# Performance work log

Measured on AMD Instinct MI355X. Metric: run time of the kernel, lower is better.

The kernel has to match this reference:

```python
import jax, jax.numpy as jnp
import numpy as np

B, S, H, T = 64, 512, 768, 400


def setup_inputs() -> dict:
    key = jax.random.key(0)
    k1, k2 = jax.random.split(key)
    hidden = jax.random.normal(k1, (B, S, H), dtype=jnp.float32)
    # word_ids: non-decreasing piece->word map per sample, like HF tokenizer word_ids()
    word_ids = jnp.sort(jax.random.randint(k2, (B, S), 0, T), axis=-1).astype(jnp.int32)
    return {"hidden": hidden, "word_ids": word_ids, "num_tokens": T}


def reference(hidden, word_ids, num_tokens):
    # Ragged segment mean-pool: pool subword pieces into per-word reps.
    # hidden: [B, S, H] float; word_ids: [B, S] int in [0, num_tokens)
    b, s, h = hidden.shape
    # Flatten (sample, word) into one global segment id: sample*T + word
    seg = (jnp.arange(b, dtype=word_ids.dtype)[:, None] * num_tokens + word_ids).reshape(-1)
    sums = jax.ops.segment_sum(hidden.reshape(b * s, h), seg, num_segments=b * num_tokens)
    counts = jax.ops.segment_sum(jnp.ones((b * s,), hidden.dtype), seg, num_segments=b * num_tokens)
    # Words with zero pieces -> sum 0 / 1 = 0, matching torch.zeros fallback
    pooled = sums / jnp.maximum(counts, 1.0)[:, None]
    return pooled.reshape(b, num_tokens, h)
```

## Files before the change

kernel.cpp:

```cpp
#include <hip/hip_runtime.h>


#define BB 64
#define SS 512
#define HH 768
#define TT 400
#define TCHUNK 16
#define NCHUNK (TT / TCHUNK)

__global__ __launch_bounds__(256) void bert_lattice_pool_kernel(
    const float* __restrict__ hidden,
    const int* __restrict__ word_ids,
    float* __restrict__ out)
{
    __shared__ int wid[SS];
    __shared__ int sstart[TCHUNK];
    __shared__ int send[TCHUNK];

    const int blk = blockIdx.x;
    const int b   = blk / NCHUNK;
    const int t0  = (blk - b * NCHUNK) * TCHUNK;

    const int tid = threadIdx.x;

    {
        const int2* src = reinterpret_cast<const int2*>(word_ids + b * SS);
        reinterpret_cast<int2*>(wid)[tid] = src[tid];
    }
    if (tid < TCHUNK) { sstart[tid] = 0; send[tid] = 0; }
    __syncthreads();

    #pragma unroll
    for (int k = 0; k < SS / 256; ++k) {
        const int s   = tid + k * 256;
        const int w   = wid[s];
        const int rel = w - t0;
        if (rel >= 0 && rel < TCHUNK) {
            if (s == 0      || wid[s - 1] != w) sstart[rel] = s;
            if (s == SS - 1 || wid[s + 1] != w) send[rel]   = s + 1;
        }
    }
    __syncthreads();

    const int wave = tid >> 6;
    const int lane = tid & 63;

    #pragma unroll
    for (int i = 0; i < TCHUNK / 4; ++i) {
        const int trel  = wave * (TCHUNK / 4) + i;
        const int start = sstart[trel];
        const int end   = send[trel];
        const int count = end - start;

        float4 acc0 = make_float4(0.f, 0.f, 0.f, 0.f);
        float4 acc1 = make_float4(0.f, 0.f, 0.f, 0.f);
        float4 acc2 = make_float4(0.f, 0.f, 0.f, 0.f);

        for (int s = start; s < end; ++s) {
            const float4* p =
                reinterpret_cast<const float4*>(hidden + ((size_t)b * SS + s) * HH);
            float4 v0 = p[lane];
            float4 v1 = p[lane + 64];
            float4 v2 = p[lane + 128];
            acc0.x += v0.x; acc0.y += v0.y; acc0.z += v0.z; acc0.w += v0.w;
            acc1.x += v1.x; acc1.y += v1.y; acc1.z += v1.z; acc1.w += v1.w;
            acc2.x += v2.x; acc2.y += v2.y; acc2.z += v2.z; acc2.w += v2.w;
        }

        const float inv = 1.0f / (float)(count > 0 ? count : 1);

        float4* o = reinterpret_cast<float4*>(out + ((size_t)b * TT + t0 + trel) * HH);
        o[lane]       = make_float4(acc0.x * inv, acc0.y * inv, acc0.z * inv, acc0.w * inv);
        o[lane + 64]  = make_float4(acc1.x * inv, acc1.y * inv, acc1.z * inv, acc1.w * inv);
        o[lane + 128] = make_float4(acc2.x * inv, acc2.y * inv, acc2.z * inv, acc2.w * inv);
    }
}

extern "C" void kernel_launch(void* const* d_in, const int* in_sizes, int n_in,
                              void* d_out, int out_size, void* d_ws, size_t ws_size,
                              hipStream_t stream) {
    (void)in_sizes; (void)n_in; (void)d_ws; (void)ws_size; (void)out_size;
    const float* hidden   = (const float*)d_in[0];
    const int*   word_ids = (const int*)d_in[1];
    float*       out      = (float*)d_out;

    dim3 grid(BB * NCHUNK);
    dim3 block(256);
    bert_lattice_pool_kernel<<<grid, block, 0, stream>>>(hidden, word_ids, out);
}
```

Measured before the change: 179.5 us.

## Stream contiguous segment span per block with one column per thread

Replaces the per-wave, per-word loop with a single pass over the block's contiguous span of pieces. Each of 192 threads owns one float4 column of the hidden dimension and emits a mean whenever a word run ends, with a one-row register prefetch. Empty words are zero-filled separately. This aims to balance work across waves regardless of word length, but it reduces loads in flight per thread and serializes across rows.

Measured after the change: 181.4 us. About the same (+1.1%).

```diff
diff --git a/kernel.cpp b/kernel.cpp
--- a/kernel.cpp
+++ b/kernel.cpp
@@ -7,8 +7,10 @@
 #define TT 400
 #define TCHUNK 16
 #define NCHUNK (TT / TCHUNK)
+#define NTHR 192
+#define H4 (HH / 4)
 
-__global__ __launch_bounds__(256) void bert_lattice_pool_kernel(
+__global__ __launch_bounds__(NTHR) void bert_lattice_pool_kernel(
     const float* __restrict__ hidden,
     const int* __restrict__ word_ids,
     float* __restrict__ out)
@@ -16,63 +18,66 @@
     __shared__ int wid[SS];
     __shared__ int sstart[TCHUNK];
     __shared__ int send[TCHUNK];
+    __shared__ int spanlo_s;
+    __shared__ int spanhi_s;
 
     const int blk = blockIdx.x;
     const int b   = blk / NCHUNK;
     const int t0  = (blk - b * NCHUNK) * TCHUNK;
-
+    const int t1  = t0 + TCHUNK;
     const int tid = threadIdx.x;
 
-    {
-        const int2* src = reinterpret_cast<const int2*>(word_ids + b * SS);
-        reinterpret_cast<int2*>(wid)[tid] = src[tid];
-    }
+    for (int i = tid; i < SS; i += NTHR) wid[i] = word_ids[b * SS + i];
     if (tid < TCHUNK) { sstart[tid] = 0; send[tid] = 0; }
+    if (tid == 0) { spanlo_s = SS; spanhi_s = 0; }
     __syncthreads();
 
-    #pragma unroll
-    for (int k = 0; k < SS / 256; ++k) {
-        const int s   = tid + k * 256;
-        const int w   = wid[s];
-        const int rel = w - t0;
-        if (rel >= 0 && rel < TCHUNK) {
-            if (s == 0      || wid[s - 1] != w) sstart[rel] = s;
-            if (s == SS - 1 || wid[s + 1] != w) send[rel]   = s + 1;
+    for (int s = tid; s < SS; s += NTHR) {
+        const int w = wid[s];
+        if (w >= t0 && w < t1) {
+            if (s == 0      || wid[s - 1] != w) sstart[w - t0] = s;
+            if (s == SS - 1 || wid[s + 1] != w) send[w - t0]   = s + 1;
+            if (s == 0      || wid[s - 1] < t0) spanlo_s = s;
         }
+        if (w < t1 && (s == SS - 1 || wid[s + 1] >= t1)) spanhi_s = s + 1;
     }
     __syncthreads();
 
-    const int wave = tid >> 6;
-    const int lane = tid & 63;
+    const int spanlo = spanlo_s;
+    const int spanhi = spanhi_s;
+
+    const float4* hbase = reinterpret_cast<const float4*>(hidden) + (size_t)b * SS * H4;
+    float4*       obase = reinterpret_cast<float4*>(out)          + (size_t)b * TT * H4;
+
+    if (spanlo < spanhi) {
+        float4 acc = make_float4(0.f, 0.f, 0.f, 0.f);
+        int run_start = spanlo;
+
+        float4 v = hbase[(size_t)spanlo * H4 + tid];
+        for (int s = spanlo; s < spanhi; ++s) {
+            const int sn = (s + 1 < spanhi) ? (s + 1) : s;
+            float4 vn = hbase[(size_t)sn * H4 + tid];
+
+            acc.x += v.x; acc.y += v.y; acc.z += v.z; acc.w += v.w;
+
+            const int w = wid[s];
+            const bool endrun = (s + 1 == spanhi) || (wid[s + 1] != w);
+            if (endrun) {
+                const float inv = 1.0f / (float)(s - run_start + 1);
+                obase[(size_t)w * H4 + tid] =
+                    make_float4(acc.x * inv, acc.y * inv, acc.z * inv, acc.w * inv);
+                acc = make_float4(0.f, 0.f, 0.f, 0.f);
+                run_start = s + 1;
+            }
+            v = vn;
+        }
+    }
 
     #pragma unroll
-    for (int i = 0; i < TCHUNK / 4; ++i) {
-        const int trel  = wave * (TCHUNK / 4) + i;
-        const int start = sstart[trel];
-        const int end   = send[trel];
-        const int count = end - start;
-
-        float4 acc0 = make_float4(0.f, 0.f, 0.f, 0.f);
-        float4 acc1 = make_float4(0.f, 0.f, 0.f, 0.f);
-        float4 acc2 = make_float4(0.f, 0.f, 0.f, 0.f);
-
-        for (int s = start; s < end; ++s) {
-            const float4* p =
-                reinterpret_cast<const float4*>(hidden + ((size_t)b * SS + s) * HH);
-            float4 v0 = p[lane];
-            float4 v1 = p[lane + 64];
-            float4 v2 = p[lane + 128];
-            acc0.x += v0.x; acc0.y += v0.y; acc0.z += v0.z; acc0.w += v0.w;
-            acc1.x += v1.x; acc1.y += v1.y; acc1.z += v1.z; acc1.w += v1.w;
-            acc2.x += v2.x; acc2.y += v2.y; acc2.z += v2.z; acc2.w += v2.w;
+    for (int rel = 0; rel < TCHUNK; ++rel) {
+        if (send[rel] == sstart[rel]) {
+            obase[(size_t)(t0 + rel) * H4 + tid] = make_float4(0.f, 0.f, 0.f, 0.f);
         }
-
-        const float inv = 1.0f / (float)(count > 0 ? count : 1);
-
-        float4* o = reinterpret_cast<float4*>(out + ((size_t)b * TT + t0 + trel) * HH);
-        o[lane]       = make_float4(acc0.x * inv, acc0.y * inv, acc0.z * inv, acc0.w * inv);
-        o[lane + 64]  = make_float4(acc1.x * inv, acc1.y * inv, acc1.z * inv, acc1.w * inv);
-        o[lane + 128] = make_float4(acc2.x * inv, acc2.y * inv, acc2.z * inv, acc2.w * inv);
     }
 }
 
@@ -85,6 +90,6 @@
     float*       out      = (float*)d_out;
 
     dim3 grid(BB * NCHUNK);
-    dim3 block(256);
+    dim3 block(NTHR);
     bert_lattice_pool_kernel<<<grid, block, 0, stream>>>(hidden, word_ids, out);
 }
```

## Split segment-table build from pooling into two kernels, one wave per word

Applied to the files above, without the earlier changes.

Moves the per-sample segment start/count computation into a separate small kernel that writes a packed table to workspace. The pooling kernel then gives each wave one (sample, word) pair, with no shared-memory setup or block-level sync, and writes outputs with nontemporal stores. The aim is to stop every block redundantly scanning word_ids and to expose more independent waves. In exchange it adds a second launch and a global table round-trip.

New measurement: 177.6 us. About the same (-1.1%).

```diff
diff --git a/kernel.cpp b/kernel.cpp
--- a/kernel.cpp
+++ b/kernel.cpp
@@ -5,86 +5,88 @@
 #define SS 512
 #define HH 768
 #define TT 400
-#define TCHUNK 16
-#define NCHUNK (TT / TCHUNK)
+#define H4 (HH / 4)
 
-__global__ __launch_bounds__(256) void bert_lattice_pool_kernel(
-    const float* __restrict__ hidden,
+typedef float f32x4 __attribute__((ext_vector_type(4)));
+
+__global__ __launch_bounds__(256) void build_table_kernel(
     const int* __restrict__ word_ids,
-    float* __restrict__ out)
+    int* __restrict__ table)
 {
     __shared__ int wid[SS];
-    __shared__ int sstart[TCHUNK];
-    __shared__ int send[TCHUNK];
+    __shared__ int sstart[TT];
+    __shared__ int send[TT];
 
-    const int blk = blockIdx.x;
-    const int b   = blk / NCHUNK;
-    const int t0  = (blk - b * NCHUNK) * TCHUNK;
-
+    const int b   = blockIdx.x;
     const int tid = threadIdx.x;
 
-    {
-        const int2* src = reinterpret_cast<const int2*>(word_ids + b * SS);
-        reinterpret_cast<int2*>(wid)[tid] = src[tid];
+    if (tid < SS / 4) {
+        reinterpret_cast<int4*>(wid)[tid] =
+            reinterpret_cast<const int4*>(word_ids + b * SS)[tid];
     }
-    if (tid < TCHUNK) { sstart[tid] = 0; send[tid] = 0; }
+    for (int t = tid; t < TT; t += 256) { sstart[t] = 0; send[t] = 0; }
     __syncthreads();
 
-    #pragma unroll
-    for (int k = 0; k < SS / 256; ++k) {
-        const int s   = tid + k * 256;
-        const int w   = wid[s];
-        const int rel = w - t0;
-        if (rel >= 0 && rel < TCHUNK) {
-            if (s == 0      || wid[s - 1] != w) sstart[rel] = s;
-            if (s == SS - 1 || wid[s + 1] != w) send[rel]   = s + 1;
-        }
+    for (int s = tid; s < SS; s += 256) {
+        const int w = wid[s];
+        if (s == 0      || wid[s - 1] != w) sstart[w] = s;
+        if (s == SS - 1 || wid[s + 1] != w) send[w]   = s + 1;
     }
     __syncthreads();
 
-    const int wave = tid >> 6;
-    const int lane = tid & 63;
+    for (int t = tid; t < TT; t += 256) {
+        const int st  = sstart[t];
+        const int cnt = send[t] - st;
+        table[b * TT + t] = st | (cnt << 16);
+    }
+}
 
-    #pragma unroll
-    for (int i = 0; i < TCHUNK / 4; ++i) {
-        const int trel  = wave * (TCHUNK / 4) + i;
-        const int start = sstart[trel];
-        const int end   = send[trel];
-        const int count = end - start;
+__global__ __launch_bounds__(256) void pool_kernel(
+    const float* __restrict__ hidden,
+    const int* __restrict__ table,
+    float* __restrict__ out)
+{
+    const int wave = threadIdx.x >> 6;
+    const int lane = threadIdx.x & 63;
+    const int bt   = blockIdx.x * 4 + wave;
+    const int b    = bt / TT;
 
-        float4 acc0 = make_float4(0.f, 0.f, 0.f, 0.f);
-        float4 acc1 = make_float4(0.f, 0.f, 0.f, 0.f);
-        float4 acc2 = make_float4(0.f, 0.f, 0.f, 0.f);
+    const int pack  = table[bt];
+    const int start = pack & 0xFFFF;
+    const int cnt   = pack >> 16;
 
-        for (int s = start; s < end; ++s) {
-            const float4* p =
-                reinterpret_cast<const float4*>(hidden + ((size_t)b * SS + s) * HH);
-            float4 v0 = p[lane];
-            float4 v1 = p[lane + 64];
-            float4 v2 = p[lane + 128];
-            acc0.x += v0.x; acc0.y += v0.y; acc0.z += v0.z; acc0.w += v0.w;
-            acc1.x += v1.x; acc1.y += v1.y; acc1.z += v1.z; acc1.w += v1.w;
-            acc2.x += v2.x; acc2.y += v2.y; acc2.z += v2.z; acc2.w += v2.w;
-        }
+    const f32x4* hrow = reinterpret_cast<const f32x4*>(hidden)
+                        + ((size_t)b * SS + start) * H4;
+    f32x4* orow = reinterpret_cast<f32x4*>(out) + (size_t)bt * H4;
 
-        const float inv = 1.0f / (float)(count > 0 ? count : 1);
+    f32x4 a0 = {0.f, 0.f, 0.f, 0.f};
+    f32x4 a1 = {0.f, 0.f, 0.f, 0.f};
+    f32x4 a2 = {0.f, 0.f, 0.f, 0.f};
 
-        float4* o = reinterpret_cast<float4*>(out + ((size_t)b * TT + t0 + trel) * HH);
-        o[lane]       = make_float4(acc0.x * inv, acc0.y * inv, acc0.z * inv, acc0.w * inv);
-        o[lane + 64]  = make_float4(acc1.x * inv, acc1.y * inv, acc1.z * inv, acc1.w * inv);
-        o[lane + 128] = make_float4(acc2.x * inv, acc2.y * inv, acc2.z * inv, acc2.w * inv);
+    for (int i = 0; i < cnt; ++i) {
+        const f32x4* p = hrow + (size_t)i * H4;
+        a0 += p[lane];
+        a1 += p[lane + 64];
+        a2 += p[lane + 128];
     }
+
+    const float inv = (cnt > 1) ? (1.0f / (float)cnt) : 1.0f;
+    a0 *= inv; a1 *= inv; a2 *= inv;
+
+    __builtin_nontemporal_store(a0, &orow[lane]);
+    __builtin_nontemporal_store(a1, &orow[lane + 64]);
+    __builtin_nontemporal_store(a2, &orow[lane + 128]);
 }
 
 extern "C" void kernel_launch(void* const* d_in, const int* in_sizes, int n_in,
                               void* d_out, int out_size, void* d_ws, size_t ws_size,
                               hipStream_t stream) {
-    (void)in_sizes; (void)n_in; (void)d_ws; (void)ws_size; (void)out_size;
+    (void)in_sizes; (void)n_in; (void)ws_size; (void)out_size;
     const float* hidden   = (const float*)d_in[0];
     const int*   word_ids = (const int*)d_in[1];
     float*       out      = (float*)d_out;
+    int*         table    = (int*)d_ws;
 
-    dim3 grid(BB * NCHUNK);
-    dim3 block(256);
-    bert_lattice_pool_kernel<<<grid, block, 0, stream>>>(hidden, word_ids, out);
+    build_table_kernel<<<dim3(BB), dim3(256), 0, stream>>>(word_ids, table);
+    pool_kernel<<<dim3(BB * TT / 4), dim3(256), 0, stream>>>(hidden, table, out);
 }
```
